# Kernel tuning notes

Hardware: AMD Instinct MI355X
Metric: run time of the kernel (lower is better)

Reference implementation:

```python
import jax, jax.numpy as jnp
import numpy as np
from jax import lax

DIM = 256
HEAD_DIM = 64          # v head dim and hedgehog dim
HEAD_DIM_QK = 64       # must equal HEAD_DIM for the module to run
NH = DIM // HEAD_DIM   # 4
EPS = 1e-6


def setup_inputs() -> dict:
    key = jax.random.key(0)
    ks = jax.random.split(key, 12)
    B, C, H, W, D = 1, DIM, 16, 16, 16
    x = jax.random.normal(ks[0], (B, C, H, W, D), dtype=jnp.float32)
    qk_dim = HEAD_DIM_QK * NH
    # 1x1x1 conv weights for q, k (qkv_bias=False)
    Wq = jax.random.normal(ks[1], (qk_dim, C), dtype=jnp.float32) * 0.02
    Wk = jax.random.normal(ks[2], (qk_dim, C), dtype=jnp.float32) * 0.02
    # depthwise 3x3x3 conv for v (groups=dim, bias=True)
    Wv = jax.random.normal(ks[3], (C, 1, 3, 3, 3), dtype=jnp.float32) * 0.1
    bv = jax.random.normal(ks[4], (C,), dtype=jnp.float32) * 0.02
    # HedgeHog linear layers (init is identity/zeros; use near-identity + noise)
    eye = jnp.eye(HEAD_DIM, dtype=jnp.float32)
    Wmq = eye * 0.5 + jax.random.normal(ks[5], (HEAD_DIM, HEAD_DIM), dtype=jnp.float32) * 0.02
    bmq = jnp.zeros((HEAD_DIM,), dtype=jnp.float32)
    Wmk = eye * 0.5 + jax.random.normal(ks[6], (HEAD_DIM, HEAD_DIM), dtype=jnp.float32) * 0.02
    bmk = jnp.zeros((HEAD_DIM,), dtype=jnp.float32)
    Wmv = eye * 0.5 + jax.random.normal(ks[7], (HEAD_DIM, HEAD_DIM), dtype=jnp.float32) * 0.02
    bmv = jnp.zeros((HEAD_DIM,), dtype=jnp.float32)
    return {"x": x, "Wq": Wq, "Wk": Wk, "Wv": Wv, "bv": bv,
            "Wmq": Wmq, "bmq": bmq, "Wmk": Wmk, "bmk": bmk,
            "Wmv": Wmv, "bmv": bmv}


def _hedgehog(z, W, b):
    # z: [B, nh, N, d] -> [B, 2*nh, N, d]; cat along HEAD axis (dim=1) as in torch code
    h = jnp.einsum('bhnd,ed->bhne', z, W) + b
    return jnp.concatenate([jnp.exp(h), jnp.exp(-h)], axis=1)


def reference(x, Wq, Wk, Wv, bv, Wmq, bmq, Wmk, bmk, Wmv, bmv):
    B, C, H, W_, D = x.shape
    N = H * W_ * D
    x2 = x.reshape(B, C, N)
    # 1x1x1 conv projections
    q = jnp.einsum('oc,bcn->bon', Wq, x2)  # [B, qk_dim, N]
    k = jnp.einsum('oc,bcn->bon', Wk, x2)
    # depthwise 3x3x3 conv for v
    v3 = lax.conv_general_dilated(
        x, Wv, window_strides=(1, 1, 1),
        padding=((1, 1), (1, 1), (1, 1)),
        dimension_numbers=('NCDHW', 'OIDHW', 'NCDHW'),
        feature_group_count=C) + bv[None, :, None, None, None]
    v = v3.reshape(B, C, N)
    # split heads, tokens-last -> tokens axis
    q1 = q.reshape(B, NH, HEAD_DIM_QK, N).transpose(0, 1, 3, 2)  # [B,nh,N,dqk]
    k1 = k.reshape(B, NH, HEAD_DIM_QK, N).transpose(0, 1, 3, 2)
    v1 = v.reshape(B, NH, HEAD_DIM, N).transpose(0, 1, 3, 2)     # [B,nh,N,dv]
    qf = _hedgehog(q1, Wmq, bmq)  # [B,2nh,N,dqk]
    kf = _hedgehog(k1, Wmk, bmk)
    vf = _hedgehog(v1, Wmv, bmv)  # [B,2nh,N,dv]
    # quadratic "linear" attention: row-sum normalized QK^T
    qk = jnp.einsum('bhmd,bhnd->bhmn', qf, kf)          # [B,2nh,N,N]
    attn = qk / (jnp.sum(qk, axis=-1, keepdims=True) + EPS)
    out = jnp.einsum('bhmn,bhnd->bhmd', attn, vf)        # [B,2nh,N,dv]
    out = out.transpose(0, 1, 3, 2).reshape(B, 2 * C, H, W_, D)
    return out
```

## Files before the change

kernel.cpp:

```cpp
#include <hip/hip_runtime.h>
#include <math.h>

#define EPS_F 1e-6f

typedef __attribute__((ext_vector_type(8))) short bf16x8;
typedef __attribute__((ext_vector_type(4))) float f32x4;

#define OFF_BV  0
#define OFF_VC  (OFF_BV + 256)
#define OFF_PS  (OFF_VC + 256*4096)
#define OFF_PSV (OFF_PS + 8*128*4096)
#define OFF_SM  (OFF_PSV + 8*128*64)
#define OFF_SV  (OFF_SM + 8*4096)
#define OFF_QF  (OFF_SV + 512)
#define OFF_WQH (OFF_QF + 512*4096)
#define OFF_WQL (OFF_WQH + 32768)
#define OFF_WKH (OFF_WQL + 32768)
#define OFF_WKL (OFF_WKH + 32768)
#define OFF_XTH (OFF_WKL + 32768)
#define OFF_XTL (OFF_XTH + 524288)

__device__ __forceinline__ void split_bf16(float v, unsigned short& h, unsigned short& l) {
    unsigned int b = __float_as_uint(v);
    h = (unsigned short)(b >> 16);
    float fh = __uint_as_float(b & 0xFFFF0000u);
    l = (unsigned short)(__float_as_uint(v - fh) >> 16);
}

__global__ __launch_bounds__(256) void k_pre(
    const float* __restrict__ x,
    const float* __restrict__ Wq, const float* __restrict__ Wk,
    const float* __restrict__ Wv, const float* __restrict__ bv,
    const float* __restrict__ Wmq, const float* __restrict__ Wmk,
    const float* __restrict__ Wmv, const float* __restrict__ bmv,
    float* __restrict__ ws)
{
    __shared__ float Ts[64][65];
    int b = blockIdx.x, t = threadIdx.x;
    if (b < 4096) {
        int c = b >> 4;
        int n = (b & 15) * 256 + t;
        int z = n >> 8, y = (n >> 4) & 15, xx = n & 15;
        const float* xc = x + c * 4096;
        const float* wc = Wv + c * 27;
        float acc = 0.f;
        #pragma unroll
        for (int kz = 0; kz < 3; ++kz) {
            int zz = z + kz - 1;
            if (zz < 0 || zz > 15) continue;
            #pragma unroll
            for (int ky = 0; ky < 3; ++ky) {
                int yy = y + ky - 1;
                if (yy < 0 || yy > 15) continue;
                #pragma unroll
                for (int kx = 0; kx < 3; ++kx) {
                    int xv = xx + kx - 1;
                    if (xv < 0 || xv > 15) continue;
                    acc = fmaf(wc[(kz*3 + ky)*3 + kx], xc[(zz << 8) + (yy << 4) + xv], acc);
                }
            }
        }
        ws[OFF_VC + (size_t)c*4096 + n] = acc;
    } else if (b < 4352) {
        int row = b - 4096, c = t;
        int h = row >> 6, e = row & 63;
        float aq = 0.f, ak = 0.f;
        for (int d = 0; d < 64; ++d) {
            float mq = Wmq[e*64 + d];
            float mk = Wmk[e*64 + d];
            int src = (h*64 + d)*256 + c;
            aq = fmaf(mq, Wq[src], aq);
            ak = fmaf(mk, Wk[src], ak);
        }
        unsigned short hh, ll;
        unsigned short* WQH = (unsigned short*)(ws + OFF_WQH);
        unsigned short* WQL = (unsigned short*)(ws + OFF_WQL);
        unsigned short* WKH = (unsigned short*)(ws + OFF_WKH);
        unsigned short* WKL = (unsigned short*)(ws + OFF_WKL);
        split_bf16(aq, hh, ll); WQH[row*256 + c] = hh; WQL[row*256 + c] = ll;
        split_bf16(ak, hh, ll); WKH[row*256 + c] = hh; WKL[row*256 + c] = ll;
        if (c == 0) {
            float av = 0.f;
            for (int d = 0; d < 64; ++d) av = fmaf(Wmv[e*64 + d], bv[h*64 + d], av);
            ws[OFF_BV + row] = av + bmv[e];
        }
    } else if (b < 4608) {
        int bx = b - 4352;
        int tx = bx & 63, cy = bx >> 6;
        int lr = t >> 6, lc2 = t & 63;
        #pragma unroll
        for (int i = 0; i < 16; ++i) {
            int row = lr*16 + i;
            Ts[row][lc2] = x[(size_t)(cy*64 + row)*4096 + tx*64 + lc2];
        }
        __syncthreads();
        int tok = t >> 2, c16 = (t & 3) * 16;
        unsigned int hw[8], lw[8];
        #pragma unroll
        for (int j = 0; j < 8; ++j) {
            float v0 = Ts[c16 + 2*j][tok], v1 = Ts[c16 + 2*j + 1][tok];
            unsigned int b0 = __float_as_uint(v0), b1 = __float_as_uint(v1);
            hw[j] = (b0 >> 16) | (b1 & 0xFFFF0000u);
            float f0 = __uint_as_float(b0 & 0xFFFF0000u);
            float f1 = __uint_as_float(b1 & 0xFFFF0000u);
            lw[j] = (__float_as_uint(v0 - f0) >> 16) | (__float_as_uint(v1 - f1) & 0xFFFF0000u);
        }
        unsigned short* XH = (unsigned short*)(ws + OFF_XTH);
        unsigned short* XL = (unsigned short*)(ws + OFF_XTL);
        size_t base = (size_t)(tx*64 + tok)*256 + cy*64 + c16;
        uint4 H0 = {hw[0], hw[1], hw[2], hw[3]}, H1 = {hw[4], hw[5], hw[6], hw[7]};
        uint4 L0 = {lw[0], lw[1], lw[2], lw[3]}, L1 = {lw[4], lw[5], lw[6], lw[7]};
        *(uint4*)(XH + base) = H0;  *(uint4*)(XH + base + 8) = H1;
        *(uint4*)(XL + base) = L0;  *(uint4*)(XL + base + 8) = L1;
    } else {
        int idx = (b - 4608)*256 + t;
        if (idx < 32768) ws[OFF_SM + idx] = 0.f;
        else             ws[OFF_SV + idx - 32768] = 0.f;
    }
}

__global__ __launch_bounds__(512, 4) void k_fused(
    const float* __restrict__ bmk, const float* __restrict__ bmq,
    const float* __restrict__ Wmv, float* __restrict__ ws)
{
    __shared__ float smem[10240];
    unsigned short* su = (unsigned short*)smem;

    int t = threadIdx.x;
    int chunk = blockIdx.x;
    int hb = blockIdx.y;
    int n0 = chunk * 32;
    int w = t >> 6, lane = t & 63;
    int kq = w >> 2;
    int wi = w & 3;
    int mh = wi & 1, nh = wi >> 1;
    int l15 = lane & 15, l4 = lane >> 4;
    bool isQ = (t >= 256);
    int tl = t & 255;

    const unsigned short* XH  = (const unsigned short*)(ws + OFF_XTH);
    const unsigned short* XL  = (const unsigned short*)(ws + OFF_XTL);
    const unsigned short* WKHp = (const unsigned short*)(ws + OFF_WKH);
    const unsigned short* WKLp = (const unsigned short*)(ws + OFF_WKL);
    const unsigned short* WQHp = (const unsigned short*)(ws + OFF_WQH);
    const unsigned short* WQLp = (const unsigned short*)(ws + OFF_WQL);

    f32x4 acc[2];
    acc[0] = (f32x4){0.f, 0.f, 0.f, 0.f};
    acc[1] = (f32x4){0.f, 0.f, 0.f, 0.f};
    float accV[2][4];
    #pragma unroll
    for (int i = 0; i < 2; ++i)
        #pragma unroll
        for (int j = 0; j < 4; ++j) accV[i][j] = 0.f;

    for (int cs = 0; cs < 4; ++cs) {
        int c0 = cs * 64;
        {
            int s = t & 7;
            int xb = t >> 8;
            int r5 = (t >> 3) & 31;
            const unsigned short* XSrc = xb ? XL : XH;
            unsigned short* xd = su + xb*2048 + r5*64 + (((s) ^ (r5 & 7)) << 3);
            *(uint4*)xd = *(const uint4*)(XSrc + (size_t)(n0 + r5)*256 + c0 + s*8);
            int r6 = (t >> 3) & 63;
            size_t wo = (size_t)(hb*64 + r6)*256 + c0 + s*8;
            unsigned short* wd0 = su + 4096 + r6*64 + (((s) ^ (r6 & 7)) << 3);
            *(uint4*)(wd0)          = *(const uint4*)(WKHp + wo);
            *(uint4*)(wd0 + 4096)   = *(const uint4*)(WKLp + wo);
            *(uint4*)(wd0 + 8192)   = *(const uint4*)(WQHp + wo);
            *(uint4*)(wd0 + 12288)  = *(const uint4*)(WQLp + wo);
        }
        __syncthreads();
        const unsigned short* Xh = su;
        const unsigned short* Xl = su + 2048;
        const unsigned short* Wh = su + 4096 + kq*8192;
        const unsigned short* Wl = Wh + 4096;
        #pragma unroll
        for (int ks = 0; ks < 2; ++ks) {
            int ar = mh*16 + l15;
            int aoff = ar*64 + (((ks*4 + l4) ^ (ar & 7)) << 3);
            bf16x8 ah = *(const bf16x8*)(Xh + aoff);
            bf16x8 al = *(const bf16x8*)(Xl + aoff);
            #pragma unroll
            for (int nt = 0; nt < 2; ++nt) {
                int br = nh*32 + nt*16 + l15;
                int boff = br*64 + (((ks*4 + l4) ^ (br & 7)) << 3);
                bf16x8 bh = *(const bf16x8*)(Wh + boff);
                bf16x8 bl = *(const bf16x8*)(Wl + boff);
                acc[nt] = __builtin_amdgcn_mfma_f32_16x16x32_bf16(ah, bh, acc[nt], 0, 0, 0);
                acc[nt] = __builtin_amdgcn_mfma_f32_16x16x32_bf16(al, bh, acc[nt], 0, 0, 0);
                acc[nt] = __builtin_amdgcn_mfma_f32_16x16x32_bf16(ah, bl, acc[nt], 0, 0, 0);
            }
        }
        __syncthreads();
    }

    float* Vs = smem;
    float* Wms = smem + 2048;
    if (!isQ) {
        const float* vcb = ws + OFF_VC + (size_t)hb*64*4096;
        #pragma unroll
        for (int i = 0; i < 8; ++i) {
            int idx = i*256 + tl;
            int row = idx >> 5, col = idx & 31;
            Vs[row*32 + col] = vcb[(size_t)row*4096 + n0 + col];
        }
        #pragma unroll
        for (int i = 0; i < 16; ++i) { int idx = i*256 + tl; Wms[(idx & 63)*68 + (idx >> 6)] = Wmv[idx]; }
    }
    __syncthreads();

    int n2 = (tl >> 4) * 2;
    int e4 = (tl & 15) * 4;
    if (!isQ) {
        #pragma unroll 4
        for (int d = 0; d < 64; ++d) {
            float x0 = Vs[d*32 + n2], x1 = Vs[d*32 + n2 + 1];
            float4 wv4 = *(const float4*)&Wms[d*68 + e4];
            float wv[4] = {wv4.x, wv4.y, wv4.z, wv4.w};
            #pragma unroll
            for (int jj = 0; jj < 4; ++jj) {
                accV[0][jj] = fmaf(x0, wv[jj], accV[0][jj]);
                accV[1][jj] = fmaf(x1, wv[jj], accV[1][jj]);
            }
        }
    }
    __syncthreads();

    float* kfp = smem;
    float* kfm = smem + 2048;
    float* vfp = smem + 4096;
    float* vfm = smem + 6144;
    if (!isQ) {
        float bk0 = bmk[nh*32 + l15], bk1 = bmk[nh*32 + 16 + l15];
        #pragma unroll
        for (int nt = 0; nt < 2; ++nt) {
            float bkv = nt ? bk1 : bk0;
            int feat = nh*32 + nt*16 + l15;
            #pragma unroll
            for (int r = 0; r < 4; ++r) {
                int tok = mh*16 + l4*4 + r;
                float v = acc[nt][r] + bkv;
                kfp[tok*64 + feat] = __expf(v);
                kfm[tok*64 + feat] = __expf(-v);
            }
        }
        float bvv[4];
        #pragma unroll
        for (int j = 0; j < 4; ++j) bvv[j] = ws[OFF_BV + hb*64 + e4 + j];
        #pragma unroll
        for (int ii = 0; ii < 2; ++ii) {
            float pv[4], mv[4];
            #pragma unroll
            for (int jj = 0; jj < 4; ++jj) {
                float bb = accV[ii][jj] + bvv[jj];
                pv[jj] = __expf(bb);  mv[jj] = __expf(-bb);
            }
            *(float4*)&vfp[(n2 + ii)*64 + e4] = make_float4(pv[0], pv[1], pv[2], pv[3]);
            *(float4*)&vfm[(n2 + ii)*64 + e4] = make_float4(mv[0], mv[1], mv[2], mv[3]);
        }
    }
    __syncthreads();

    float aSp[4][4], aSm[4][4], svp[4], svm[4];
    #pragma unroll
    for (int i = 0; i < 4; ++i) {
        svp[i] = 0.f; svm[i] = 0.f;
        #pragma unroll
        for (int j = 0; j < 4; ++j) { aSp[i][j] = 0.f; aSm[i][j] = 0.f; }
    }
    int a4 = (tl & 15) * 4, f4 = (tl >> 4) * 4;
    int nb = isQ ? 16 : 0;
    #pragma unroll 2
    for (int nn = 0; nn < 16; ++nn) {
        int n = nb + nn;
        float4 kp4 = *(const float4*)&kfp[n*64 + a4];
        float4 km4 = *(const float4*)&kfm[n*64 + a4];
        float4 vp4 = *(const float4*)&vfp[n*64 + f4];
        float4 vm4 = *(const float4*)&vfm[n*64 + f4];
        float kp[4] = {kp4.x, kp4.y, kp4.z, kp4.w};
        float km[4] = {km4.x, km4.y, km4.z, km4.w};
        float vp[4] = {vp4.x, vp4.y, vp4.z, vp4.w};
        float vm[4] = {vm4.x, vm4.y, vm4.z, vm4.w};
        #pragma unroll
        for (int ai = 0; ai < 4; ++ai) {
            svp[ai] += kp[ai];  svm[ai] += km[ai];
            #pragma unroll
            for (int fi = 0; fi < 4; ++fi) {
                aSp[ai][fi] = fmaf(kp[ai], vp[fi], aSp[ai][fi]);
                aSm[ai][fi] = fmaf(km[ai], vm[fi], aSm[ai][fi]);
            }
        }
    }
    __syncthreads();

    if (isQ) {
        #pragma unroll
        for (int i = 0; i < 4; ++i)
            #pragma unroll
            for (int j = 0; j < 4; ++j) {
                smem[(i*4 + j)*256 + tl]      = aSp[i][j];
                smem[(16 + i*4 + j)*256 + tl] = aSm[i][j];
            }
        if (tl < 16) {
            #pragma unroll
            for (int i = 0; i < 4; ++i) {
                smem[8192 + i*16 + tl]      = svp[i];
                smem[8192 + 64 + i*16 + tl] = svm[i];
            }
        }
    }
    __syncthreads();
    if (!isQ) {
        #pragma unroll
        for (int i = 0; i < 4; ++i)
            #pragma unroll
            for (int j = 0; j < 4; ++j) {
                aSp[i][j] += smem[(i*4 + j)*256 + tl];
                aSm[i][j] += smem[(16 + i*4 + j)*256 + tl];
            }
        float* pSp = ws + OFF_PS + (size_t)(hb*128 + chunk)*4096;
        float* pSm = ws + OFF_PS + (size_t)((hb + 4)*128 + chunk)*4096;
        #pragma unroll
        for (int ai = 0; ai < 4; ++ai) {
            *(float4*)&pSp[(a4 + ai)*64 + f4] = make_float4(aSp[ai][0], aSp[ai][1], aSp[ai][2], aSp[ai][3]);
            *(float4*)&pSm[(a4 + ai)*64 + f4] = make_float4(aSm[ai][0], aSm[ai][1], aSm[ai][2], aSm[ai][3]);
        }
        if (tl < 16) {
            #pragma unroll
            for (int i = 0; i < 4; ++i) {
                svp[i] += smem[8192 + i*16 + tl];
                svm[i] += smem[8192 + 64 + i*16 + tl];
            }
            float* pvp = ws + OFF_PSV + (size_t)(hb*128 + chunk)*64;
            float* pvm = ws + OFF_PSV + (size_t)((hb + 4)*128 + chunk)*64;
            *(float4*)&pvp[a4] = make_float4(svp[0], svp[1], svp[2], svp[3]);
            *(float4*)&pvm[a4] = make_float4(svm[0], svm[1], svm[2], svm[3]);
        }
    }
    __syncthreads();

    float* qTp = smem;
    float* qTm = smem + 2304;
    if (isQ) {
        float bq0 = bmq[nh*32 + l15], bq1 = bmq[nh*32 + 16 + l15];
        #pragma unroll
        for (int nt = 0; nt < 2; ++nt) {
            float bqv = nt ? bq1 : bq0;
            int feat = nh*32 + nt*16 + l15;
            #pragma unroll
            for (int r = 0; r < 4; ++r) {
                int tok = mh*16 + l4*4 + r;
                float v = acc[nt][r] + bqv;
                qTp[feat*36 + tok] = __expf(v);
                qTm[feat*36 + tok] = __expf(-v);
            }
        }
    }
    __syncthreads();
    float* gq = ws + OFF_QF;
    #pragma unroll
    for (int j = 0; j < 2; ++j) {
        int un = t + 512*j;
        int s = un >> 9;
        int rem = un & 511;
        int feat = rem >> 3, t4 = (rem & 7) * 4;
        const float* src = (s ? &qTm[feat*36 + t4] : &qTp[feat*36 + t4]);
        float4 v = *(const float4*)src;
        *(float4*)&gq[(size_t)((hb + 4*s)*64 + feat)*4096 + n0 + t4] = v;
    }
}

__global__ __launch_bounds__(256) void k_reduce(float* __restrict__ ws)
{
    int tid = blockIdx.x*256 + threadIdx.x;
    if (tid < 131072) {
        int part = tid >> 15;
        int o = tid & 32767;
        int h = o >> 12, r = o & 4095;
        float s = 0.f;
        #pragma unroll 8
        for (int c = 0; c < 32; ++c)
            s += ws[OFF_PS + (size_t)(h*128 + part*32 + c)*4096 + r];
        atomicAdd(&ws[OFF_SM + o], s);
    } else if (tid < 131072 + 2048) {
        int j = tid - 131072;
        int part = j >> 9;
        int o = j & 511;
        int h = o >> 6, e = o & 63;
        float s = 0.f;
        #pragma unroll 8
        for (int c = 0; c < 32; ++c)
            s += ws[OFF_PSV + (size_t)(h*128 + part*32 + c)*64 + e];
        atomicAdd(&ws[OFF_SV + o], s);
    }
}

__global__ __launch_bounds__(256, 6) void k_out(
    const float* __restrict__ ws, float* __restrict__ out)
{
    __shared__ float qs[64][32];
    __shared__ float Sms[64][64];
    __shared__ float svs[64];
    int t = threadIdx.x;
    int cx = blockIdx.x;
    int h = blockIdx.y;
    int n0 = cx * 32;

    const float* gq = ws + OFF_QF + (size_t)h*64*4096;
    #pragma unroll
    for (int i = 0; i < 8; ++i) {
        int idx = i*256 + t;
        qs[idx >> 5][idx & 31] = gq[(size_t)(idx >> 5)*4096 + n0 + (idx & 31)];
    }
    const float* Smg = ws + OFF_SM + (size_t)h*4096;
    #pragma unroll
    for (int i = 0; i < 16; ++i) { int idx = i*256 + t; Sms[idx >> 6][idx & 63] = Smg[idx]; }
    if (t < 64) svs[t] = ws[OFF_SV + h*64 + t];
    __syncthreads();

    int e2 = (t >> 3) * 2;
    int n4 = (t & 7) * 4;
    float acc[2][4];
    float den[4] = {0.f, 0.f, 0.f, 0.f};
    #pragma unroll
    for (int i = 0; i < 2; ++i)
        #pragma unroll
        for (int j = 0; j < 4; ++j) acc[i][j] = 0.f;
    #pragma unroll 4
    for (int a = 0; a < 64; ++a) {
        float4 qv4 = *(const float4*)&qs[a][n4];
        float qv[4] = {qv4.x, qv4.y, qv4.z, qv4.w};
        float sm0 = Sms[a][e2], sm1 = Sms[a][e2 + 1];
        float sva = svs[a];
        #pragma unroll
        for (int nj = 0; nj < 4; ++nj) {
            den[nj] = fmaf(qv[nj], sva, den[nj]);
            acc[0][nj] = fmaf(sm0, qv[nj], acc[0][nj]);
            acc[1][nj] = fmaf(sm1, qv[nj], acc[1][nj]);
        }
    }
    float r[4];
    #pragma unroll
    for (int nj = 0; nj < 4; ++nj) r[nj] = 1.f / (den[nj] + EPS_F);
    #pragma unroll
    for (int ei = 0; ei < 2; ++ei)
        *(float4*)&out[(size_t)(h*64 + e2 + ei)*4096 + n0 + n4] =
            make_float4(acc[ei][0]*r[0], acc[ei][1]*r[1], acc[ei][2]*r[2], acc[ei][3]*r[3]);
}

extern "C" void kernel_launch(void* const* d_in, const int* in_sizes, int n_in,
                              void* d_out, int out_size, void* d_ws, size_t ws_size,
                              hipStream_t stream) {
    const float* x   = (const float*)d_in[0];
    const float* Wq  = (const float*)d_in[1];
    const float* Wk  = (const float*)d_in[2];
    const float* Wv  = (const float*)d_in[3];
    const float* bv  = (const float*)d_in[4];
    const float* Wmq = (const float*)d_in[5];
    const float* bmq = (const float*)d_in[6];
    const float* Wmk = (const float*)d_in[7];
    const float* bmk = (const float*)d_in[8];
    const float* Wmv = (const float*)d_in[9];
    const float* bmv = (const float*)d_in[10];
    float* out = (float*)d_out;
    float* ws  = (float*)d_ws;

    k_pre<<<4738, 256, 0, stream>>>(x, Wq, Wk, Wv, bv, Wmq, Wmk, Wmv, bmv, ws);
    k_fused<<<dim3(128, 4), 512, 0, stream>>>(bmk, bmq, Wmv, ws);
    k_reduce<<<521, 256, 0, stream>>>(ws);
    k_out<<<dim3(128, 8), 256, 0, stream>>>(ws, out);
}
```

Before: 127.6 us.

## Move Q projection and hedgehog feature map from k_fused into k_out

The Q projection MFMA and its exp feature map move out of the key/value state kernel into the output kernel, so qf is no longer written to and reread from global workspace. k_fused drops to 256 threads handling K/V only, with each thread covering all 32 tokens instead of splitting tokens between two thread halves and merging through shared memory. k_out now recomputes Q from the bf16 split inputs and handles both +/- heads per block, with half the grid. This removes the qf round trip, but k_out gets longer and k_fused loses parallelism.

```diff
diff --git a/kernel.cpp b/kernel.cpp
--- a/kernel.cpp
+++ b/kernel.cpp
@@ -119,11 +119,11 @@
     }
 }
 
-__global__ __launch_bounds__(512, 4) void k_fused(
-    const float* __restrict__ bmk, const float* __restrict__ bmq,
-    const float* __restrict__ Wmv, float* __restrict__ ws)
+__global__ __launch_bounds__(256, 4) void k_fused(
+    const float* __restrict__ bmk, const float* __restrict__ Wmv,
+    float* __restrict__ ws)
 {
-    __shared__ float smem[10240];
+    __shared__ float smem[8192];
     unsigned short* su = (unsigned short*)smem;
 
     int t = threadIdx.x;
@@ -131,19 +131,13 @@
     int hb = blockIdx.y;
     int n0 = chunk * 32;
     int w = t >> 6, lane = t & 63;
-    int kq = w >> 2;
-    int wi = w & 3;
-    int mh = wi & 1, nh = wi >> 1;
+    int mh = w & 1, nh = w >> 1;
     int l15 = lane & 15, l4 = lane >> 4;
-    bool isQ = (t >= 256);
-    int tl = t & 255;
 
     const unsigned short* XH  = (const unsigned short*)(ws + OFF_XTH);
     const unsigned short* XL  = (const unsigned short*)(ws + OFF_XTL);
     const unsigned short* WKHp = (const unsigned short*)(ws + OFF_WKH);
     const unsigned short* WKLp = (const unsigned short*)(ws + OFF_WKL);
-    const unsigned short* WQHp = (const unsigned short*)(ws + OFF_WQH);
-    const unsigned short* WQLp = (const unsigned short*)(ws + OFF_WQL);
 
     f32x4 acc[2];
     acc[0] = (f32x4){0.f, 0.f, 0.f, 0.f};
@@ -156,26 +150,27 @@
 
     for (int cs = 0; cs < 4; ++cs) {
         int c0 = cs * 64;
-        {
-            int s = t & 7;
-            int xb = t >> 8;
-            int r5 = (t >> 3) & 31;
+        #pragma unroll
+        for (int i = 0; i < 2; ++i) {
+            int u = t + 256*i;
+            int xb = u >> 8, r5 = (u >> 3) & 31, s = u & 7;
             const unsigned short* XSrc = xb ? XL : XH;
-            unsigned short* xd = su + xb*2048 + r5*64 + (((s) ^ (r5 & 7)) << 3);
-            *(uint4*)xd = *(const uint4*)(XSrc + (size_t)(n0 + r5)*256 + c0 + s*8);
-            int r6 = (t >> 3) & 63;
-            size_t wo = (size_t)(hb*64 + r6)*256 + c0 + s*8;
-            unsigned short* wd0 = su + 4096 + r6*64 + (((s) ^ (r6 & 7)) << 3);
-            *(uint4*)(wd0)          = *(const uint4*)(WKHp + wo);
-            *(uint4*)(wd0 + 4096)   = *(const uint4*)(WKLp + wo);
-            *(uint4*)(wd0 + 8192)   = *(const uint4*)(WQHp + wo);
-            *(uint4*)(wd0 + 12288)  = *(const uint4*)(WQLp + wo);
+            *(uint4*)(su + xb*2048 + r5*64 + ((s ^ (r5 & 7)) << 3)) =
+                *(const uint4*)(XSrc + (size_t)(n0 + r5)*256 + c0 + s*8);
+        }
+        #pragma unroll
+        for (int i = 0; i < 4; ++i) {
+            int u = t + 256*i;
+            int wb = u >> 9, r6 = (u >> 3) & 63, s = u & 7;
+            const unsigned short* WSrc = wb ? WKLp : WKHp;
+            *(uint4*)(su + 4096 + wb*4096 + r6*64 + ((s ^ (r6 & 7)) << 3)) =
+                *(const uint4*)(WSrc + (size_t)(hb*64 + r6)*256 + c0 + s*8);
         }
         __syncthreads();
         const unsigned short* Xh = su;
         const unsigned short* Xl = su + 2048;
-        const unsigned short* Wh = su + 4096 + kq*8192;
-        const unsigned short* Wl = Wh + 4096;
+        const unsigned short* Wh = su + 4096;
+        const unsigned short* Wl = su + 8192;
         #pragma unroll
         for (int ks = 0; ks < 2; ++ks) {
             int ar = mh*16 + l15;
@@ -198,32 +193,30 @@
 
     float* Vs = smem;
     float* Wms = smem + 2048;
-    if (!isQ) {
+    {
         const float* vcb = ws + OFF_VC + (size_t)hb*64*4096;
         #pragma unroll
         for (int i = 0; i < 8; ++i) {
-            int idx = i*256 + tl;
+            int idx = i*256 + t;
             int row = idx >> 5, col = idx & 31;
             Vs[row*32 + col] = vcb[(size_t)row*4096 + n0 + col];
         }
         #pragma unroll
-        for (int i = 0; i < 16; ++i) { int idx = i*256 + tl; Wms[(idx & 63)*68 + (idx >> 6)] = Wmv[idx]; }
+        for (int i = 0; i < 16; ++i) { int idx = i*256 + t; Wms[(idx & 63)*68 + (idx >> 6)] = Wmv[idx]; }
     }
     __syncthreads();
 
-    int n2 = (tl >> 4) * 2;
-    int e4 = (tl & 15) * 4;
-    if (!isQ) {
-        #pragma unroll 4
-        for (int d = 0; d < 64; ++d) {
-            float x0 = Vs[d*32 + n2], x1 = Vs[d*32 + n2 + 1];
-            float4 wv4 = *(const float4*)&Wms[d*68 + e4];
-            float wv[4] = {wv4.x, wv4.y, wv4.z, wv4.w};
-            #pragma unroll
-            for (int jj = 0; jj < 4; ++jj) {
-                accV[0][jj] = fmaf(x0, wv[jj], accV[0][jj]);
-                accV[1][jj] = fmaf(x1, wv[jj], accV[1][jj]);
-            }
+    int n2 = (t >> 4) * 2;
+    int e4 = (t & 15) * 4;
+    #pragma unroll 4
+    for (int d = 0; d < 64; ++d) {
+        float x0 = Vs[d*32 + n2], x1 = Vs[d*32 + n2 + 1];
+        float4 wv4 = *(const float4*)&Wms[d*68 + e4];
+        float wv[4] = {wv4.x, wv4.y, wv4.z, wv4.w};
+        #pragma unroll
+        for (int jj = 0; jj < 4; ++jj) {
+            accV[0][jj] = fmaf(x0, wv[jj], accV[0][jj]);
+            accV[1][jj] = fmaf(x1, wv[jj], accV[1][jj]);
         }
     }
     __syncthreads();
@@ -232,7 +225,7 @@
     float* kfm = smem + 2048;
     float* vfp = smem + 4096;
     float* vfm = smem + 6144;
-    if (!isQ) {
+    {
         float bk0 = bmk[nh*32 + l15], bk1 = bmk[nh*32 + 16 + l15];
         #pragma unroll
         for (int nt = 0; nt < 2; ++nt) {
@@ -270,11 +263,9 @@
         #pragma unroll
         for (int j = 0; j < 4; ++j) { aSp[i][j] = 0.f; aSm[i][j] = 0.f; }
     }
-    int a4 = (tl & 15) * 4, f4 = (tl >> 4) * 4;
-    int nb = isQ ? 16 : 0;
+    int a4 = (t & 15) * 4, f4 = (t >> 4) * 4;
     #pragma unroll 2
-    for (int nn = 0; nn < 16; ++nn) {
-        int n = nb + nn;
+    for (int n = 0; n < 32; ++n) {
         float4 kp4 = *(const float4*)&kfp[n*64 + a4];
         float4 km4 = *(const float4*)&kfm[n*64 + a4];
         float4 vp4 = *(const float4*)&vfp[n*64 + f4];
@@ -293,82 +284,18 @@
             }
         }
     }
-    __syncthreads();
-
-    if (isQ) {
-        #pragma unroll
-        for (int i = 0; i < 4; ++i)
-            #pragma unroll
-            for (int j = 0; j < 4; ++j) {
-                smem[(i*4 + j)*256 + tl]      = aSp[i][j];
-                smem[(16 + i*4 + j)*256 + tl] = aSm[i][j];
-            }
-        if (tl < 16) {
-            #pragma unroll
-            for (int i = 0; i < 4; ++i) {
-                smem[8192 + i*16 + tl]      = svp[i];
-                smem[8192 + 64 + i*16 + tl] = svm[i];
-            }
-        }
-    }
-    __syncthreads();
-    if (!isQ) {
-        #pragma unroll
-        for (int i = 0; i < 4; ++i)
-            #pragma unroll
-            for (int j = 0; j < 4; ++j) {
-                aSp[i][j] += smem[(i*4 + j)*256 + tl];
-                aSm[i][j] += smem[(16 + i*4 + j)*256 + tl];
-            }
-        float* pSp = ws + OFF_PS + (size_t)(hb*128 + chunk)*4096;
-        float* pSm = ws + OFF_PS + (size_t)((hb + 4)*128 + chunk)*4096;
-        #pragma unroll
-        for (int ai = 0; ai < 4; ++ai) {
-            *(float4*)&pSp[(a4 + ai)*64 + f4] = make_float4(aSp[ai][0], aSp[ai][1], aSp[ai][2], aSp[ai][3]);
-            *(float4*)&pSm[(a4 + ai)*64 + f4] = make_float4(aSm[ai][0], aSm[ai][1], aSm[ai][2], aSm[ai][3]);
-        }
-        if (tl < 16) {
-            #pragma unroll
-            for (int i = 0; i < 4; ++i) {
-                svp[i] += smem[8192 + i*16 + tl];
-                svm[i] += smem[8192 + 64 + i*16 + tl];
-            }
-            float* pvp = ws + OFF_PSV + (size_t)(hb*128 + chunk)*64;
-            float* pvm = ws + OFF_PSV + (size_t)((hb + 4)*128 + chunk)*64;
-            *(float4*)&pvp[a4] = make_float4(svp[0], svp[1], svp[2], svp[3]);
-            *(float4*)&pvm[a4] = make_float4(svm[0], svm[1], svm[2], svm[3]);
-        }
-    }
-    __syncthreads();
-
-    float* qTp = smem;
-    float* qTm = smem + 2304;
-    if (isQ) {
-        float bq0 = bmq[nh*32 + l15], bq1 = bmq[nh*32 + 16 + l15];
-        #pragma unroll
-        for (int nt = 0; nt < 2; ++nt) {
-            float bqv = nt ? bq1 : bq0;
-            int feat = nh*32 + nt*16 + l15;
-            #pragma unroll
-            for (int r = 0; r < 4; ++r) {
-                int tok = mh*16 + l4*4 + r;
-                float v = acc[nt][r] + bqv;
-                qTp[feat*36 + tok] = __expf(v);
-                qTm[feat*36 + tok] = __expf(-v);
-            }
-        }
-    }
-    __syncthreads();
-    float* gq = ws + OFF_QF;
+    float* pSp = ws + OFF_PS + (size_t)(hb*128 + chunk)*4096;
+    float* pSm = ws + OFF_PS + (size_t)((hb + 4)*128 + chunk)*4096;
     #pragma unroll
-    for (int j = 0; j < 2; ++j) {
-        int un = t + 512*j;
-        int s = un >> 9;
-        int rem = un & 511;
-        int feat = rem >> 3, t4 = (rem & 7) * 4;
-        const float* src = (s ? &qTm[feat*36 + t4] : &qTp[feat*36 + t4]);
-        float4 v = *(const float4*)src;
-        *(float4*)&gq[(size_t)((hb + 4*s)*64 + feat)*4096 + n0 + t4] = v;
+    for (int ai = 0; ai < 4; ++ai) {
+        *(float4*)&pSp[(a4 + ai)*64 + f4] = make_float4(aSp[ai][0], aSp[ai][1], aSp[ai][2], aSp[ai][3]);
+        *(float4*)&pSm[(a4 + ai)*64 + f4] = make_float4(aSm[ai][0], aSm[ai][1], aSm[ai][2], aSm[ai][3]);
+    }
+    if (t < 16) {
+        float* pvp = ws + OFF_PSV + (size_t)(hb*128 + chunk)*64;
+        float* pvm = ws + OFF_PSV + (size_t)((hb + 4)*128 + chunk)*64;
+        *(float4*)&pvp[a4] = make_float4(svp[0], svp[1], svp[2], svp[3]);
+        *(float4*)&pvm[a4] = make_float4(svm[0], svm[1], svm[2], svm[3]);
     }
 }
 
@@ -397,57 +324,132 @@
     }
 }
 
-__global__ __launch_bounds__(256, 6) void k_out(
-    const float* __restrict__ ws, float* __restrict__ out)
+__global__ __launch_bounds__(256, 4) void k_out(
+    const float* __restrict__ bmq, const float* __restrict__ ws,
+    float* __restrict__ out)
 {
-    __shared__ float qs[64][32];
-    __shared__ float Sms[64][64];
-    __shared__ float svs[64];
+    __shared__ float smem[8768];
+    unsigned short* su = (unsigned short*)smem;
+
     int t = threadIdx.x;
     int cx = blockIdx.x;
-    int h = blockIdx.y;
+    int hb = blockIdx.y;
     int n0 = cx * 32;
-
-    const float* gq = ws + OFF_QF + (size_t)h*64*4096;
-    #pragma unroll
-    for (int i = 0; i < 8; ++i) {
-        int idx = i*256 + t;
-        qs[idx >> 5][idx & 31] = gq[(size_t)(idx >> 5)*4096 + n0 + (idx & 31)];
-    }
-    const float* Smg = ws + OFF_SM + (size_t)h*4096;
-    #pragma unroll
-    for (int i = 0; i < 16; ++i) { int idx = i*256 + t; Sms[idx >> 6][idx & 63] = Smg[idx]; }
-    if (t < 64) svs[t] = ws[OFF_SV + h*64 + t];
-    __syncthreads();
-
+    int w = t >> 6, lane = t & 63;
+    int mh = w & 1, nh = w >> 1;
+    int l15 = lane & 15, l4 = lane >> 4;
+
+    const unsigned short* XH  = (const unsigned short*)(ws + OFF_XTH);
+    const unsigned short* XL  = (const unsigned short*)(ws + OFF_XTL);
+    const unsigned short* WQHp = (const unsigned short*)(ws + OFF_WQH);
+    const unsigned short* WQLp = (const unsigned short*)(ws + OFF_WQL);
+
+    f32x4 acc[2];
+    acc[0] = (f32x4){0.f, 0.f, 0.f, 0.f};
+    acc[1] = (f32x4){0.f, 0.f, 0.f, 0.f};
+
+    for (int cs = 0; cs < 4; ++cs) {
+        int c0 = cs * 64;
+        #pragma unroll
+        for (int i = 0; i < 2; ++i) {
+            int u = t + 256*i;
+            int xb = u >> 8, r5 = (u >> 3) & 31, s = u & 7;
+            const unsigned short* XSrc = xb ? XL : XH;
+            *(uint4*)(su + xb*2048 + r5*64 + ((s ^ (r5 & 7)) << 3)) =
+                *(const uint4*)(XSrc + (size_t)(n0 + r5)*256 + c0 + s*8);
+        }
+        #pragma unroll
+        for (int i = 0; i < 4; ++i) {
+            int u = t + 256*i;
+            int wb = u >> 9, r6 = (u >> 3) & 63, s = u & 7;
+            const unsigned short* WSrc = wb ? WQLp : WQHp;
+            *(uint4*)(su + 4096 + wb*4096 + r6*64 + ((s ^ (r6 & 7)) << 3)) =
+                *(const uint4*)(WSrc + (size_t)(hb*64 + r6)*256 + c0 + s*8);
+        }
+        __syncthreads();
+        const unsigned short* Xh = su;
+        const unsigned short* Xl = su + 2048;
+        const unsigned short* Wh = su + 4096;
+        const unsigned short* Wl = su + 8192;
+        #pragma unroll
+        for (int ks = 0; ks < 2; ++ks) {
+            int ar = mh*16 + l15;
+            int aoff = ar*64 + (((ks*4 + l4) ^ (ar & 7)) << 3);
+            bf16x8 ah = *(const bf16x8*)(Xh + aoff);
+            bf16x8 al = *(const bf16x8*)(Xl + aoff);
+            #pragma unroll
+            for (int nt = 0; nt < 2; ++nt) {
+                int br = nh*32 + nt*16 + l15;
+                int boff = br*64 + (((ks*4 + l4) ^ (br & 7)) << 3);
+                bf16x8 bh = *(const bf16x8*)(Wh + boff);
+                bf16x8 bl = *(const bf16x8*)(Wl + boff);
+                acc[nt] = __builtin_amdgcn_mfma_f32_16x16x32_bf16(ah, bh, acc[nt], 0, 0, 0);
+                acc[nt] = __builtin_amdgcn_mfma_f32_16x16x32_bf16(al, bh, acc[nt], 0, 0, 0);
+                acc[nt] = __builtin_amdgcn_mfma_f32_16x16x32_bf16(ah, bl, acc[nt], 0, 0, 0);
+            }
+        }
+        __syncthreads();
+    }
+
+    float* qTp = smem;
+    float* qTm = smem + 2304;
+    {
+        float bq0 = bmq[nh*32 + l15], bq1 = bmq[nh*32 + 16 + l15];
+        #pragma unroll
+        for (int nt = 0; nt < 2; ++nt) {
+            float bqv = nt ? bq1 : bq0;
+            int feat = nh*32 + nt*16 + l15;
+            #pragma unroll
+            for (int r = 0; r < 4; ++r) {
+                int tok = mh*16 + l4*4 + r;
+                float v = acc[nt][r] + bqv;
+                qTp[feat*36 + tok] = __expf(v);
+                qTm[feat*36 + tok] = __expf(-v);
+            }
+        }
+    }
+
+    float* Sms = smem + 4608;
+    float* svs = smem + 8704;
     int e2 = (t >> 3) * 2;
     int n4 = (t & 7) * 4;
-    float acc[2][4];
-    float den[4] = {0.f, 0.f, 0.f, 0.f};
-    #pragma unroll
-    for (int i = 0; i < 2; ++i)
-        #pragma unroll
-        for (int j = 0; j < 4; ++j) acc[i][j] = 0.f;
-    #pragma unroll 4
-    for (int a = 0; a < 64; ++a) {
-        float4 qv4 = *(const float4*)&qs[a][n4];
-        float qv[4] = {qv4.x, qv4.y, qv4.z, qv4.w};
-        float sm0 = Sms[a][e2], sm1 = Sms[a][e2 + 1];
-        float sva = svs[a];
-        #pragma unroll
-        for (int nj = 0; nj < 4; ++nj) {
-            den[nj] = fmaf(qv[nj], sva, den[nj]);
-            acc[0][nj] = fmaf(sm0, qv[nj], acc[0][nj]);
-            acc[1][nj] = fmaf(sm1, qv[nj], acc[1][nj]);
-        }
-    }
-    float r[4];
-    #pragma unroll
-    for (int nj = 0; nj < 4; ++nj) r[nj] = 1.f / (den[nj] + EPS_F);
-    #pragma unroll
-    for (int ei = 0; ei < 2; ++ei)
-        *(float4*)&out[(size_t)(h*64 + e2 + ei)*4096 + n0 + n4] =
-            make_float4(acc[ei][0]*r[0], acc[ei][1]*r[1], acc[ei][2]*r[2], acc[ei][3]*r[3]);
+    for (int s = 0; s < 2; ++s) {
+        int h = hb + 4*s;
+        __syncthreads();
+        const float* Smg = ws + OFF_SM + (size_t)h*4096;
+        #pragma unroll
+        for (int i = 0; i < 16; ++i) { int idx = i*256 + t; Sms[idx] = Smg[idx]; }
+        if (t < 64) svs[t] = ws[OFF_SV + h*64 + t];
+        __syncthreads();
+
+        const float* qs = s ? qTm : qTp;
+        float acc2[2][4];
+        float den[4] = {0.f, 0.f, 0.f, 0.f};
+        #pragma unroll
+        for (int i = 0; i < 2; ++i)
+            #pragma unroll
+            for (int j = 0; j < 4; ++j) acc2[i][j] = 0.f;
+        #pragma unroll 4
+        for (int a = 0; a < 64; ++a) {
+            float4 qv4 = *(const float4*)&qs[a*36 + n4];
+            float qv[4] = {qv4.x, qv4.y, qv4.z, qv4.w};
+            float sm0 = Sms[a*64 + e2], sm1 = Sms[a*64 + e2 + 1];
+            float sva = svs[a];
+            #pragma unroll
+            for (int nj = 0; nj < 4; ++nj) {
+                den[nj] = fmaf(qv[nj], sva, den[nj]);
+                acc2[0][nj] = fmaf(sm0, qv[nj], acc2[0][nj]);
+                acc2[1][nj] = fmaf(sm1, qv[nj], acc2[1][nj]);
+            }
+        }
+        float r[4];
+        #pragma unroll
+        for (int nj = 0; nj < 4; ++nj) r[nj] = 1.f / (den[nj] + EPS_F);
+        #pragma unroll
+        for (int ei = 0; ei < 2; ++ei)
+            *(float4*)&out[(size_t)(h*64 + e2 + ei)*4096 + n0 + n4] =
+                make_float4(acc2[ei][0]*r[0], acc2[ei][1]*r[1], acc2[ei][2]*r[2], acc2[ei][3]*r[3]);
+    }
 }
 
 extern "C" void kernel_launch(void* const* d_in, const int* in_sizes, int n_in,
@@ -468,7 +470,7 @@
     float* ws  = (float*)d_ws;
 
     k_pre<<<4738, 256, 0, stream>>>(x, Wq, Wk, Wv, bv, Wmq, Wmk, Wmv, bmv, ws);
-    k_fused<<<dim3(128, 4), 512, 0, stream>>>(bmk, bmq, Wmv, ws);
+    k_fused<<<dim3(128, 4), 256, 0, stream>>>(bmk, Wmv, ws);
     k_reduce<<<521, 256, 0, stream>>>(ws);
-    k_out<<<dim3(128, 8), 256, 0, stream>>>(ws, out);
-}
+    k_out<<<dim3(128, 4), 256, 0, stream>>>(bmq, ws, out);
+}
```

Measured after the change: 128.1 us. No clear change (+0.4%).
